# Kernel tuning notes

Hardware: AMD Instinct MI355X
Metric: run time of the kernel (lower is better)

## Reference

```python
import jax, jax.numpy as jnp
import numpy as np

N = 784        # input_size == output_size
C = 2          # connections_per_neuron
NUM_CLASSES = 10


def _column_index_map():
    """Faithful reproduction of the torch loop's scatter targets.

    For i < 782: layer i writes out[:,0] -> col i, out[:,1] -> col i+1.
    For i = 782: wraparound branch with cutoff=0 writes to cols (0, 1).
    For i = 783: cutoff=1 writes out[:,0] -> col 783, out[:,1] -> col 0.
    """
    i = np.arange(N)
    col0 = i.copy()
    col1 = (i + 1) % N
    col0[N - 2] = 0   # i = 782 buggy wraparound in original code
    col1[N - 2] = 1
    return jnp.asarray(np.stack([col0, col1], axis=1))  # [784, 2] int32


def setup_inputs() -> dict:
    key = jax.random.key(0)
    k1, k2, k3, k4, k5 = jax.random.split(key, 5)
    B = 65536
    bound_sp = 1.0  # Linear(1,2): bound = 1/sqrt(1)
    bound_fc = 1.0 / np.sqrt(N)
    return {
        "x": jax.random.normal(k1, (B, N), dtype=jnp.float32),
        # stacked Linear(1,2) params: W_sparse[i,k] = weight of layer i, output k
        "W_sparse": jax.random.uniform(k2, (N, C), jnp.float32, -bound_sp, bound_sp),
        "b_sparse": jax.random.uniform(k3, (N, C), jnp.float32, -bound_sp, bound_sp),
        "fc_w": jax.random.uniform(k4, (NUM_CLASSES, N), jnp.float32, -bound_fc, bound_fc),
        "fc_b": jax.random.uniform(k5, (NUM_CLASSES,), jnp.float32, -bound_fc, bound_fc),
    }


def reference(x, W_sparse, b_sparse, fc_w, fc_b):
    B = x.shape[0]
    x = x.reshape(B, -1)                                   # [B, 784]
    # all 784 tiny Linear(1,2) calls at once: [B, 784, 2]
    contrib = x[:, :, None] * W_sparse[None] + b_sparse[None]
    idx = _column_index_map()                              # [784, 2]
    y = jnp.zeros((B, N), dtype=x.dtype).at[:, idx].add(contrib)
    logits = y @ fc_w.T + fc_b                             # [B, 10]
    return jax.nn.softmax(logits, axis=-1)
```

## Files before the change

kernel.cpp:

```cpp
#include <hip/hip_runtime.h>

#define N_FEAT 784
#define NF4    196
#define N_CLS  10

__global__ __launch_bounds__(256, 4) void sparse_fused_kernel(
    const float* __restrict__ x,
    const float* __restrict__ Wsp,
    const float* __restrict__ bsp,
    const float* __restrict__ fcw,
    const float* __restrict__ fcb,
    float* __restrict__ out)
{
    __shared__ float Wl[N_CLS * N_FEAT];
    __shared__ float bl[N_CLS];
    __shared__ float bred[4][N_CLS];

    const int tid  = threadIdx.x;
    const int lane = tid & 63;
    const int wave = tid >> 6;

    float bacc[N_CLS];
#pragma unroll
    for (int n = 0; n < N_CLS; ++n) bacc[n] = 0.f;

    for (int i = tid; i < N_FEAT; i += 256) {
        int c0 = (i == 782) ? 0 : i;
        int c1 = (i == 782) ? 1 : ((i == 783) ? 0 : (i + 1));
        float w0 = Wsp[2 * i], w1 = Wsp[2 * i + 1];
        float b0 = bsp[2 * i], b1 = bsp[2 * i + 1];
#pragma unroll
        for (int n = 0; n < N_CLS; ++n) {
            float f0 = fcw[n * N_FEAT + c0];
            float f1 = fcw[n * N_FEAT + c1];
            Wl[n * N_FEAT + i] = f0 * w0 + f1 * w1;
            bacc[n] += f0 * b0 + f1 * b1;
        }
    }
#pragma unroll
    for (int n = 0; n < N_CLS; ++n) {
#pragma unroll
        for (int d = 1; d < 64; d <<= 1)
            bacc[n] += __shfl_xor(bacc[n], d, 64);
    }
    if (lane == 0) {
#pragma unroll
        for (int n = 0; n < N_CLS; ++n) bred[wave][n] = bacc[n];
    }
    __syncthreads();
    if (tid < N_CLS)
        bl[tid] = bred[0][tid] + bred[1][tid] + bred[2][tid] + bred[3][tid] + fcb[tid];
    __syncthreads();

    const float4* Wl4 = (const float4*)Wl;
    const int gw = blockIdx.x * 4 + wave;
    const int g  = lane >> 4;
    const int sl = lane & 15;

#pragma unroll
    for (int pass = 0; pass < 2; ++pass) {
        const int rbase = (gw * 2 + pass) * 8 + g * 2;
        const float4* xr0 = (const float4*)(x + (size_t)rbase * N_FEAT);
        const float4* xr1 = (const float4*)(x + (size_t)(rbase + 1) * N_FEAT);

        float acc0[N_CLS], acc1[N_CLS];
#pragma unroll
        for (int n = 0; n < N_CLS; ++n) { acc0[n] = 0.f; acc1[n] = 0.f; }

        for (int k4 = sl; k4 < NF4; k4 += 16) {
            float4 x0 = xr0[k4];
            float4 x1 = xr1[k4];
#pragma unroll
            for (int n = 0; n < N_CLS; ++n) {
                float4 wv = Wl4[n * NF4 + k4];
                acc0[n] += wv.x * x0.x + wv.y * x0.y + wv.z * x0.z + wv.w * x0.w;
                acc1[n] += wv.x * x1.x + wv.y * x1.y + wv.z * x1.z + wv.w * x1.w;
            }
        }

#pragma unroll
        for (int d = 1; d < 16; d <<= 1) {
#pragma unroll
            for (int n = 0; n < N_CLS; ++n) {
                acc0[n] += __shfl_xor(acc0[n], d, 64);
                acc1[n] += __shfl_xor(acc1[n], d, 64);
            }
        }

        float m0 = -1e30f, m1 = -1e30f;
#pragma unroll
        for (int n = 0; n < N_CLS; ++n) {
            acc0[n] += bl[n];
            acc1[n] += bl[n];
            m0 = fmaxf(m0, acc0[n]);
            m1 = fmaxf(m1, acc1[n]);
        }
        float den0 = 0.f, den1 = 0.f;
#pragma unroll
        for (int n = 0; n < N_CLS; ++n) {
            acc0[n] = __expf(acc0[n] - m0);
            acc1[n] = __expf(acc1[n] - m1);
            den0 += acc0[n];
            den1 += acc1[n];
        }
        float inv0 = 1.0f / den0, inv1 = 1.0f / den1;
        float v0 = acc0[0], v1 = acc1[0];
#pragma unroll
        for (int n = 1; n < N_CLS; ++n) {
            v0 = (sl == n) ? acc0[n] : v0;
            v1 = (sl == n) ? acc1[n] : v1;
        }
        if (sl < N_CLS) {
            out[(size_t)rbase * N_CLS + sl]       = v0 * inv0;
            out[(size_t)(rbase + 1) * N_CLS + sl] = v1 * inv1;
        }
    }
}

extern "C" void kernel_launch(void* const* d_in, const int* in_sizes, int n_in,
                              void* d_out, int out_size, void* d_ws, size_t ws_size,
                              hipStream_t stream) {
    const float* x   = (const float*)d_in[0];
    const float* Wsp = (const float*)d_in[1];
    const float* bsp = (const float*)d_in[2];
    const float* fcw = (const float*)d_in[3];
    const float* fcb = (const float*)d_in[4];
    float* out = (float*)d_out;

    sparse_fused_kernel<<<1024, 256, 0, stream>>>(x, Wsp, bsp, fcw, fcb, out);
}
```

Baseline: 294.3 us.

## Use 512-thread blocks with one pass per wave and split the k-loop

Doubles the block size to 8 waves so each wave handles one group of 8 rows in a single pass instead of two sequential passes, keeping the grid at 1024 blocks. The shared fused weight matrix is built once per block and amortized across 64 rows using twice as many threads. The reduction loop is split into 12 full iterations plus a 4-lane tail, so the main loop has a fixed trip count the compiler can unroll. In exchange the launch bound of 512x8 constrains registers per thread, and the setup phase gives fewer rows of work per thread.

```diff
diff --git a/kernel.cpp b/kernel.cpp
--- a/kernel.cpp
+++ b/kernel.cpp
@@ -4,7 +4,7 @@
 #define NF4    196
 #define N_CLS  10
 
-__global__ __launch_bounds__(256, 4) void sparse_fused_kernel(
+__global__ __launch_bounds__(512, 8) void sparse_fused_kernel(
     const float* __restrict__ x,
     const float* __restrict__ Wsp,
     const float* __restrict__ bsp,
@@ -14,7 +14,7 @@
 {
     __shared__ float Wl[N_CLS * N_FEAT];
     __shared__ float bl[N_CLS];
-    __shared__ float bred[4][N_CLS];
+    __shared__ float bred[8][N_CLS];
 
     const int tid  = threadIdx.x;
     const int lane = tid & 63;
@@ -24,7 +24,7 @@
 #pragma unroll
     for (int n = 0; n < N_CLS; ++n) bacc[n] = 0.f;
 
-    for (int i = tid; i < N_FEAT; i += 256) {
+    for (int i = tid; i < N_FEAT; i += 512) {
         int c0 = (i == 782) ? 0 : i;
         int c1 = (i == 782) ? 1 : ((i == 783) ? 0 : (i + 1));
         float w0 = Wsp[2 * i], w1 = Wsp[2 * i + 1];
@@ -48,72 +48,83 @@
         for (int n = 0; n < N_CLS; ++n) bred[wave][n] = bacc[n];
     }
     __syncthreads();
-    if (tid < N_CLS)
-        bl[tid] = bred[0][tid] + bred[1][tid] + bred[2][tid] + bred[3][tid] + fcb[tid];
+    if (tid < N_CLS) {
+        float s = fcb[tid];
+#pragma unroll
+        for (int w = 0; w < 8; ++w) s += bred[w][tid];
+        bl[tid] = s;
+    }
     __syncthreads();
 
     const float4* Wl4 = (const float4*)Wl;
-    const int gw = blockIdx.x * 4 + wave;
     const int g  = lane >> 4;
     const int sl = lane & 15;
 
+    const int rbase = blockIdx.x * 64 + wave * 8 + g * 2;
+    const float4* xr = (const float4*)(x + (size_t)rbase * N_FEAT);
+
+    float acc0[N_CLS], acc1[N_CLS];
 #pragma unroll
-    for (int pass = 0; pass < 2; ++pass) {
-        const int rbase = (gw * 2 + pass) * 8 + g * 2;
-        const float4* xr0 = (const float4*)(x + (size_t)rbase * N_FEAT);
-        const float4* xr1 = (const float4*)(x + (size_t)(rbase + 1) * N_FEAT);
+    for (int n = 0; n < N_CLS; ++n) { acc0[n] = 0.f; acc1[n] = 0.f; }
 
-        float acc0[N_CLS], acc1[N_CLS];
+    for (int i = 0; i < 12; ++i) {
+        const int k4 = sl + 16 * i;
+        float4 x0 = xr[k4];
+        float4 x1 = xr[NF4 + k4];
 #pragma unroll
-        for (int n = 0; n < N_CLS; ++n) { acc0[n] = 0.f; acc1[n] = 0.f; }
-
-        for (int k4 = sl; k4 < NF4; k4 += 16) {
-            float4 x0 = xr0[k4];
-            float4 x1 = xr1[k4];
+        for (int n = 0; n < N_CLS; ++n) {
+            float4 wv = Wl4[n * NF4 + k4];
+            acc0[n] += wv.x * x0.x + wv.y * x0.y + wv.z * x0.z + wv.w * x0.w;
+            acc1[n] += wv.x * x1.x + wv.y * x1.y + wv.z * x1.z + wv.w * x1.w;
+        }
+    }
+    if (sl < 4) {
+        const int k4 = 192 + sl;
+        float4 x0 = xr[k4];
+        float4 x1 = xr[NF4 + k4];
 #pragma unroll
-            for (int n = 0; n < N_CLS; ++n) {
-                float4 wv = Wl4[n * NF4 + k4];
-                acc0[n] += wv.x * x0.x + wv.y * x0.y + wv.z * x0.z + wv.w * x0.w;
-                acc1[n] += wv.x * x1.x + wv.y * x1.y + wv.z * x1.z + wv.w * x1.w;
-            }
+        for (int n = 0; n < N_CLS; ++n) {
+            float4 wv = Wl4[n * NF4 + k4];
+            acc0[n] += wv.x * x0.x + wv.y * x0.y + wv.z * x0.z + wv.w * x0.w;
+            acc1[n] += wv.x * x1.x + wv.y * x1.y + wv.z * x1.z + wv.w * x1.w;
         }
+    }
 
 #pragma unroll
-        for (int d = 1; d < 16; d <<= 1) {
-#pragma unroll
-            for (int n = 0; n < N_CLS; ++n) {
-                acc0[n] += __shfl_xor(acc0[n], d, 64);
-                acc1[n] += __shfl_xor(acc1[n], d, 64);
-            }
-        }
-
-        float m0 = -1e30f, m1 = -1e30f;
+    for (int d = 1; d < 16; d <<= 1) {
 #pragma unroll
         for (int n = 0; n < N_CLS; ++n) {
-            acc0[n] += bl[n];
-            acc1[n] += bl[n];
-            m0 = fmaxf(m0, acc0[n]);
-            m1 = fmaxf(m1, acc1[n]);
+            acc0[n] += __shfl_xor(acc0[n], d, 64);
+            acc1[n] += __shfl_xor(acc1[n], d, 64);
         }
-        float den0 = 0.f, den1 = 0.f;
+    }
+
+    float m0 = -1e30f, m1 = -1e30f;
 #pragma unroll
-        for (int n = 0; n < N_CLS; ++n) {
-            acc0[n] = __expf(acc0[n] - m0);
-            acc1[n] = __expf(acc1[n] - m1);
-            den0 += acc0[n];
-            den1 += acc1[n];
-        }
-        float inv0 = 1.0f / den0, inv1 = 1.0f / den1;
-        float v0 = acc0[0], v1 = acc1[0];
+    for (int n = 0; n < N_CLS; ++n) {
+        acc0[n] += bl[n];
+        acc1[n] += bl[n];
+        m0 = fmaxf(m0, acc0[n]);
+        m1 = fmaxf(m1, acc1[n]);
+    }
+    float den0 = 0.f, den1 = 0.f;
 #pragma unroll
-        for (int n = 1; n < N_CLS; ++n) {
-            v0 = (sl == n) ? acc0[n] : v0;
-            v1 = (sl == n) ? acc1[n] : v1;
-        }
-        if (sl < N_CLS) {
-            out[(size_t)rbase * N_CLS + sl]       = v0 * inv0;
-            out[(size_t)(rbase + 1) * N_CLS + sl] = v1 * inv1;
-        }
+    for (int n = 0; n < N_CLS; ++n) {
+        acc0[n] = __expf(acc0[n] - m0);
+        acc1[n] = __expf(acc1[n] - m1);
+        den0 += acc0[n];
+        den1 += acc1[n];
+    }
+    float inv0 = 1.0f / den0, inv1 = 1.0f / den1;
+    float v0 = acc0[0], v1 = acc1[0];
+#pragma unroll
+    for (int n = 1; n < N_CLS; ++n) {
+        v0 = (sl == n) ? acc0[n] : v0;
+        v1 = (sl == n) ? acc1[n] : v1;
+    }
+    if (sl < N_CLS) {
+        out[(size_t)rbase * N_CLS + sl]       = v0 * inv0;
+        out[(size_t)(rbase + 1) * N_CLS + sl] = v1 * inv1;
     }
 }
 
@@ -127,5 +138,5 @@
     const float* fcb = (const float*)d_in[4];
     float* out = (float*)d_out;
 
-    sparse_fused_kernel<<<1024, 256, 0, stream>>>(x, Wsp, bsp, fcw, fcb, out);
+    sparse_fused_kernel<<<1024, 512, 0, stream>>>(x, Wsp, bsp, fcw, fcb, out);
 }
```

Result: slower. 308.2 us (+4.7%).
